# Optimization experiments

Hardware: AMD Instinct MI355X
Metric: run time of the kernel (lower is better)

Reference implementation:

```python
import jax, jax.numpy as jnp
import numpy as np
from jax import lax

DIM = 64
NUM_HEADS = 1
HEAD_DIM = DIM // NUM_HEADS
SR = 8  # reduction_ratio
SCALE = HEAD_DIM ** -0.5


def setup_inputs() -> dict:
    key = jax.random.key(0)
    ks = jax.random.split(key, 12)
    s = 0.02
    return {
        "x": jax.random.normal(ks[0], (8, 16384, DIM), dtype=jnp.float32),
        # conv sr: (out_ch, in_ch, kH, kW) torch OIHW layout
        "sr_w": jax.random.normal(ks[1], (DIM, DIM, SR, SR), dtype=jnp.float32) * s,
        "sr_b": jnp.zeros((DIM,), jnp.float32),
        "ln_g": jnp.ones((DIM,), jnp.float32),
        "ln_b": jnp.zeros((DIM,), jnp.float32),
        # torch Linear weights: (out_features, in_features)
        "q_w": jax.random.normal(ks[2], (DIM, DIM), dtype=jnp.float32) * s,
        "q_b": jnp.zeros((DIM,), jnp.float32),
        "kv_w": jax.random.normal(ks[3], (2 * DIM, DIM), dtype=jnp.float32) * s,
        "kv_b": jnp.zeros((2 * DIM,), jnp.float32),
        "proj_w": jax.random.normal(ks[4], (DIM, DIM), dtype=jnp.float32) * s,
        "proj_b": jnp.zeros((DIM,), jnp.float32),
    }


def _layernorm(x, g, b, eps=1e-5):
    mu = jnp.mean(x, axis=-1, keepdims=True)
    var = jnp.var(x, axis=-1, keepdims=True)
    return (x - mu) * lax.rsqrt(var + eps) * g + b


def reference(x, sr_w, sr_b, ln_g, ln_b, q_w, q_b, kv_w, kv_b, proj_w, proj_b):
    B, N, C = x.shape
    H = W = int(N ** 0.5)
    # q: (B, heads, N, head_dim)
    q = (x @ q_w.T + q_b).reshape(B, N, NUM_HEADS, HEAD_DIM).transpose(0, 2, 1, 3)
    # spatial reduction of KV via strided conv + LayerNorm
    x_ = x.transpose(0, 2, 1).reshape(B, C, H, W)
    x_ = lax.conv_general_dilated(
        x_, sr_w, window_strides=(SR, SR), padding="VALID",
        dimension_numbers=("NCHW", "OIHW", "NCHW"))
    x_ = x_ + sr_b[None, :, None, None]
    x_ = x_.reshape(B, C, -1).transpose(0, 2, 1)  # (B, Nr, C)
    x_ = _layernorm(x_, ln_g, ln_b)
    Nr = x_.shape[1]
    kv = (x_ @ kv_w.T + kv_b).reshape(B, Nr, 2, NUM_HEADS, HEAD_DIM)
    kv = kv.transpose(2, 0, 3, 1, 4)  # (2, B, heads, Nr, hd)
    k, v = kv[0], kv[1]
    attn = jnp.einsum("bhnd,bhmd->bhnm", q, k) * SCALE
    attn = jax.nn.softmax(attn, axis=-1)
    out = jnp.einsum("bhnm,bhmd->bhnd", attn, v)
    out = out.transpose(0, 2, 1, 3).reshape(B, N, C)
    return out @ proj_w.T + proj_b
```

## Files before the change

### kernel.cpp

```cpp
#include <hip/hip_runtime.h>


typedef __attribute__((ext_vector_type(8))) short bf16x8;
typedef __attribute__((ext_vector_type(4))) float f32x4;

__device__ __forceinline__ unsigned short f2bf(float f) {
    union { float f; unsigned int u; } a; a.f = f;
    unsigned int r = a.u + 0x7FFFu + ((a.u >> 16) & 1u);
    return (unsigned short)(r >> 16);
}
__device__ __forceinline__ float bf2f(unsigned short h) {
    union { unsigned int u; float f; } a; a.u = ((unsigned int)h) << 16;
    return a.f;
}
union U8 { uint4 u; bf16x8 v; };
__device__ __forceinline__ bf16x8 pack8(float e0,float e1,float e2,float e3,
                                        float e4,float e5,float e6,float e7){
    U8 r;
    r.u.x = (unsigned)f2bf(e0) | ((unsigned)f2bf(e1)<<16);
    r.u.y = (unsigned)f2bf(e2) | ((unsigned)f2bf(e3)<<16);
    r.u.z = (unsigned)f2bf(e4) | ((unsigned)f2bf(e5)<<16);
    r.u.w = (unsigned)f2bf(e6) | ((unsigned)f2bf(e7)<<16);
    return r.v;
}
__device__ __forceinline__ bf16x8 ldg8(const unsigned short* p){
    U8 r; r.u = *(const uint4*)p; return r.v;
}

__global__ __launch_bounds__(256) void prep_kernel(
    const float* __restrict__ sr_w, const float* __restrict__ sr_b,
    const float* __restrict__ q_w, const float* __restrict__ q_b,
    const float* __restrict__ proj_w,
    unsigned short* __restrict__ wbp, float* __restrict__ conv_out,
    unsigned short* __restrict__ qwb, unsigned short* __restrict__ pwph,
    unsigned short* __restrict__ pwpl, float* __restrict__ qb_s)
{
    int tid = blockIdx.x * 256 + threadIdx.x;
    {
        int i = tid & 7, n = (tid>>3)&15, g = (tid>>7)&3, ks = (tid>>9)&31,
            kc = (tid>>14)&3, w = tid>>16;
        int co = 16*w + n;
        int k  = kc*1024 + ks*32 + 8*g + i;
        int kh = k >> 9, kw = (k>>6)&7, cin = k & 63;
        wbp[tid] = f2bf(sr_w[co*4096 + cin*64 + kh*8 + kw]);
    }
    if (tid < 131072) conv_out[tid] = sr_b[tid & 63];
    if (tid < 4096)   qwb[tid] = f2bf(q_w[tid] * 0.125f);
    if (tid < 4096) {
        int i = tid & 7, g = (tid>>3)&3, s3 = (tid>>5)&1, co = tid>>6;
        int ch = 32*s3 + 16*(i>>2) + 4*g + (i&3);
        float w = proj_w[co*64 + ch];
        unsigned short h = f2bf(w);
        pwph[tid] = h;
        pwpl[tid] = f2bf(w - bf2f(h));
    }
    if (tid < 64) qb_s[tid] = q_b[tid] * 0.125f;
}

__global__ __launch_bounds__(256) void conv_kernel(
    const float* __restrict__ x, const unsigned short* __restrict__ wbp,
    float* __restrict__ conv_out)
{
    __shared__ char xsm[32768];
    int bid = blockIdx.x;
    int kc = bid & 3, oh = (bid>>2) & 15, b = bid >> 6;
    int t = threadIdx.x;

    const float* slab = x + ((size_t)(b*128 + oh*8 + kc*2)) * 128 * 64;
    #pragma unroll
    for (int c2 = 0; c2 < 8; ++c2) {
        int eo = (c2*256 + t) * 8;
        float4 v0 = *(const float4*)(slab + eo);
        float4 v1 = *(const float4*)(slab + eo + 4);
        int byte = eo * 2;
        int dst = byte ^ (((byte >> 10) & 7) << 4);
        U8 tmp; tmp.v = pack8(v0.x,v0.y,v0.z,v0.w,v1.x,v1.y,v1.z,v1.w);
        *(uint4*)(xsm + dst) = tmp.u;
    }
    __syncthreads();

    int w = t >> 6, lane = t & 63, g = lane >> 4, n = lane & 15;
    f32x4 acc = {0.f, 0.f, 0.f, 0.f};
    const unsigned short* wslice = wbp + (size_t)((w*4 + kc) * 32) * 512;
    int swz = (n & 7) << 4;
    #pragma unroll
    for (int ks = 0; ks < 32; ++ks) {
        bf16x8 A = ldg8(wslice + ((ks*4 + g)*16 + n) * 8);
        int byte = (ks >> 4) * 16384 + n * 1024 + ((ks & 15) * 32 + 8*g) * 2;
        U8 Bx; Bx.u = *(const uint4*)(xsm + (byte ^ swz));
        acc = __builtin_amdgcn_mfma_f32_16x16x32_bf16(A, Bx.v, acc, 0, 0, 0);
    }
    int pos = b*256 + oh*16 + n;
    int co  = 16*w + 4*g;
    #pragma unroll
    for (int r = 0; r < 4; ++r)
        atomicAdd(&conv_out[pos*64 + co + r], acc[r]);
}

__global__ __launch_bounds__(64) void lnkv_kernel(
    const float* __restrict__ conv_out,
    const float* __restrict__ ln_g, const float* __restrict__ ln_b,
    const float* __restrict__ kv_w, const float* __restrict__ kv_b,
    unsigned short* __restrict__ kbuf, unsigned short* __restrict__ vp)
{
    int gblk = blockIdx.x;
    int b = gblk >> 8, m = gblk & 255;
    int c = threadIdx.x;
    float val = conv_out[gblk*64 + c];
    float s = val, s2 = val*val;
    #pragma unroll
    for (int o = 32; o >= 1; o >>= 1) {
        s  += __shfl_xor(s,  o, 64);
        s2 += __shfl_xor(s2, o, 64);
    }
    float mean = s * (1.f/64.f);
    float var  = s2 * (1.f/64.f) - mean*mean;
    float y = (val - mean) * rsqrtf(var + 1e-5f) * ln_g[c] + ln_b[c];
    __shared__ float ys[64];
    ys[c] = y;
    __syncthreads();
    #pragma unroll
    for (int h = 0; h < 2; ++h) {
        int oc = c + h*64;
        float acc = kv_b[oc];
        const float* wr = kv_w + oc*64;
        #pragma unroll
        for (int j = 0; j < 64; j += 4) {
            float4 w4 = *(const float4*)(wr + j);
            acc += ys[j]*w4.x + ys[j+1]*w4.y + ys[j+2]*w4.z + ys[j+3]*w4.w;
        }
        if (h == 0) {
            kbuf[(b*256 + m)*64 + c] = f2bf(acc);
        } else {
            int ks = m >> 5, hi = (m >> 4) & 1, g2 = (m >> 2) & 3, r = m & 3;
            vp[(size_t)b*16384 + ((ks*4 + g2)*64 + c)*8 + r + 4*hi] = f2bf(acc);
        }
    }
}

__global__ __launch_bounds__(256) void attn_kernel(
    const float* __restrict__ x,
    const unsigned short* __restrict__ qwb, const float* __restrict__ qb_s,
    const unsigned short* __restrict__ kbuf, const unsigned short* __restrict__ vp,
    const unsigned short* __restrict__ pwph, const unsigned short* __restrict__ pwpl,
    const float* __restrict__ proj_b,
    float* __restrict__ out)
{
    __shared__ char Ks[32768];
    __shared__ char Vs[32768];
    int bid = blockIdx.x;
    int b = bid >> 8, rt = bid & 255;
    int t = threadIdx.x;
    {
        const char* kb = (const char*)(kbuf + (size_t)b*16384);
        const char* vb = (const char*)(vp   + (size_t)b*16384);
        #pragma unroll
        for (int c = 0; c < 8; ++c) {
            int off = (c*256 + t) * 16;
            int dst = off ^ (((off >> 7) & 7) << 4);
            *(uint4*)(Ks + dst) = *(const uint4*)(kb + off);
            *(uint4*)(Vs + off) = *(const uint4*)(vb + off);
        }
    }
    __syncthreads();

    int w = t >> 6, lane = t & 63, g = lane >> 4, n = lane & 15;
    int qrow = rt*64 + w*16 + n;
    const float* xr = x + ((size_t)b*16384 + qrow) * 64;

    f32x4 qacc[4];
    #pragma unroll
    for (int tau = 0; tau < 4; ++tau)
        qacc[tau] = *(const f32x4*)(qb_s + 16*tau + 4*g);
    bf16x8 xq[2];
    #pragma unroll
    for (int s = 0; s < 2; ++s) {
        float4 v0 = *(const float4*)(xr + 32*s + 8*g);
        float4 v1 = *(const float4*)(xr + 32*s + 8*g + 4);
        xq[s] = pack8(v0.x,v0.y,v0.z,v0.w,v1.x,v1.y,v1.z,v1.w);
    }
    #pragma unroll
    for (int tau = 0; tau < 4; ++tau)
        #pragma unroll
        for (int s = 0; s < 2; ++s) {
            bf16x8 A = ldg8(qwb + (16*tau + n)*64 + 32*s + 8*g);
            qacc[tau] = __builtin_amdgcn_mfma_f32_16x16x32_bf16(A, xq[s], qacc[tau], 0,0,0);
        }
    bf16x8 qkB[2];
    #pragma unroll
    for (int s2 = 0; s2 < 2; ++s2)
        qkB[s2] = pack8(qacc[2*s2][0],  qacc[2*s2][1],  qacc[2*s2][2],  qacc[2*s2][3],
                        qacc[2*s2+1][0],qacc[2*s2+1][1],qacc[2*s2+1][2],qacc[2*s2+1][3]);

    float S[16][4];
    #pragma unroll
    for (int tt = 0; tt < 16; ++tt) {
        f32x4 sa = {0.f, 0.f, 0.f, 0.f};
        int m = 16*tt + n;
        int base = m * 128;
        int swz = (m & 7) << 4;
        #pragma unroll
        for (int s2 = 0; s2 < 2; ++s2) {
            int c1 = (32*s2 + 4*g) * 2;
            uint2 d0 = *(const uint2*)(Ks + ((base + c1)      ^ swz));
            uint2 d1 = *(const uint2*)(Ks + ((base + c1 + 32) ^ swz));
            U8 A; A.u = make_uint4(d0.x, d0.y, d1.x, d1.y);
            sa = __builtin_amdgcn_mfma_f32_16x16x32_bf16(A.v, qkB[s2], sa, 0,0,0);
        }
        S[tt][0]=sa[0]; S[tt][1]=sa[1]; S[tt][2]=sa[2]; S[tt][3]=sa[3];
    }

    float rm[16];
    #pragma unroll
    for (int tt = 0; tt < 16; ++tt)
        rm[tt] = fmaxf(fmaxf(S[tt][0],S[tt][1]), fmaxf(S[tt][2],S[tt][3]));
    float m8[8];
    #pragma unroll
    for (int j = 0; j < 8; ++j) m8[j] = fmaxf(rm[2*j], rm[2*j+1]);
    float mx = fmaxf(fmaxf(fmaxf(m8[0],m8[1]),fmaxf(m8[2],m8[3])),
                     fmaxf(fmaxf(m8[4],m8[5]),fmaxf(m8[6],m8[7])));
    mx = fmaxf(mx, __shfl_xor(mx, 16, 64));
    mx = fmaxf(mx, __shfl_xor(mx, 32, 64));
    #pragma unroll
    for (int tt = 0; tt < 16; ++tt)
        #pragma unroll
        for (int r = 0; r < 4; ++r)
            S[tt][r] = __expf(S[tt][r] - mx);
    float rs[16];
    #pragma unroll
    for (int tt = 0; tt < 16; ++tt) rs[tt] = (S[tt][0]+S[tt][1]) + (S[tt][2]+S[tt][3]);
    float s8[8];
    #pragma unroll
    for (int j = 0; j < 8; ++j) s8[j] = rs[2*j] + rs[2*j+1];
    float ssum = ((s8[0]+s8[1])+(s8[2]+s8[3])) + ((s8[4]+s8[5])+(s8[6]+s8[7]));
    ssum += __shfl_xor(ssum, 16, 64);
    ssum += __shfl_xor(ssum, 32, 64);
    float inv = 1.f / ssum;

    f32x4 oacc[4] = {{0,0,0,0},{0,0,0,0},{0,0,0,0},{0,0,0,0}};
    #pragma unroll
    for (int ks = 0; ks < 8; ++ks) {
        bf16x8 Bp = pack8(S[2*ks][0]*inv,  S[2*ks][1]*inv,  S[2*ks][2]*inv,  S[2*ks][3]*inv,
                          S[2*ks+1][0]*inv,S[2*ks+1][1]*inv,S[2*ks+1][2]*inv,S[2*ks+1][3]*inv);
        #pragma unroll
        for (int tc = 0; tc < 4; ++tc) {
            U8 A; A.u = *(const uint4*)(Vs + ((ks*4 + g)*64 + 16*tc + n) * 16);
            oacc[tc] = __builtin_amdgcn_mfma_f32_16x16x32_bf16(A.v, Bp, oacc[tc], 0,0,0);
        }
    }

    U8 BhU[2], BlU[2];
    #pragma unroll
    for (int s3 = 0; s3 < 2; ++s3) {
        unsigned short hb[8], lb[8];
        #pragma unroll
        for (int j = 0; j < 8; ++j) {
            float v = oacc[2*s3 + (j>>2)][j&3];
            hb[j] = f2bf(v);
            lb[j] = f2bf(v - bf2f(hb[j]));
        }
        BhU[s3].u.x = (unsigned)hb[0] | ((unsigned)hb[1]<<16);
        BhU[s3].u.y = (unsigned)hb[2] | ((unsigned)hb[3]<<16);
        BhU[s3].u.z = (unsigned)hb[4] | ((unsigned)hb[5]<<16);
        BhU[s3].u.w = (unsigned)hb[6] | ((unsigned)hb[7]<<16);
        BlU[s3].u.x = (unsigned)lb[0] | ((unsigned)lb[1]<<16);
        BlU[s3].u.y = (unsigned)lb[2] | ((unsigned)lb[3]<<16);
        BlU[s3].u.z = (unsigned)lb[4] | ((unsigned)lb[5]<<16);
        BlU[s3].u.w = (unsigned)lb[6] | ((unsigned)lb[7]<<16);
    }
    f32x4 pacc[4];
    #pragma unroll
    for (int tf = 0; tf < 4; ++tf)
        pacc[tf] = *(const f32x4*)(proj_b + 16*tf + 4*g);
    #pragma unroll
    for (int tf = 0; tf < 4; ++tf)
        #pragma unroll
        for (int s3 = 0; s3 < 2; ++s3) {
            bf16x8 Ah = ldg8(pwph + (((16*tf + n)*2 + s3)*4 + g)*8);
            bf16x8 Al = ldg8(pwpl + (((16*tf + n)*2 + s3)*4 + g)*8);
            pacc[tf] = __builtin_amdgcn_mfma_f32_16x16x32_bf16(Ah, BhU[s3].v, pacc[tf], 0,0,0);
            pacc[tf] = __builtin_amdgcn_mfma_f32_16x16x32_bf16(Ah, BlU[s3].v, pacc[tf], 0,0,0);
            pacc[tf] = __builtin_amdgcn_mfma_f32_16x16x32_bf16(Al, BhU[s3].v, pacc[tf], 0,0,0);
        }
    float* orow = out + ((size_t)b*16384 + qrow) * 64;
    #pragma unroll
    for (int tf = 0; tf < 4; ++tf)
        *(float4*)(orow + 16*tf + 4*g) = *(float4*)&pacc[tf];
}

extern "C" void kernel_launch(void* const* d_in, const int* in_sizes, int n_in,
                              void* d_out, int out_size, void* d_ws, size_t ws_size,
                              hipStream_t stream)
{
    const float* x      = (const float*)d_in[0];
    const float* sr_w   = (const float*)d_in[1];
    const float* sr_b   = (const float*)d_in[2];
    const float* ln_g   = (const float*)d_in[3];
    const float* ln_b   = (const float*)d_in[4];
    const float* q_w    = (const float*)d_in[5];
    const float* q_b    = (const float*)d_in[6];
    const float* kv_w   = (const float*)d_in[7];
    const float* kv_b   = (const float*)d_in[8];
    const float* proj_w = (const float*)d_in[9];
    const float* proj_b = (const float*)d_in[10];
    float* out = (float*)d_out;

    char* wsb = (char*)d_ws;
    unsigned short* wbp  = (unsigned short*)(wsb);
    float*          conv = (float*)(wsb + 524288);
    unsigned short* kbuf = (unsigned short*)(wsb + 1048576);
    unsigned short* vp   = (unsigned short*)(wsb + 1310720);
    unsigned short* qwb  = (unsigned short*)(wsb + 1572864);
    unsigned short* pwph = (unsigned short*)(wsb + 1581056);
    unsigned short* pwpl = (unsigned short*)(wsb + 1589248);
    float*          qb_s = (float*)(wsb + 1597440);

    hipLaunchKernelGGL(prep_kernel, dim3(1024), dim3(256), 0, stream,
                       sr_w, sr_b, q_w, q_b, proj_w, wbp, conv, qwb, pwph, pwpl, qb_s);
    hipLaunchKernelGGL(conv_kernel, dim3(512), dim3(256), 0, stream, x, wbp, conv);
    hipLaunchKernelGGL(lnkv_kernel, dim3(2048), dim3(64), 0, stream,
                       conv, ln_g, ln_b, kv_w, kv_b, kbuf, vp);
    hipLaunchKernelGGL(attn_kernel, dim3(2048), dim3(256), 0, stream,
                       x, qwb, qb_s, kbuf, vp, pwph, pwpl, proj_b, out);
}
```

Baseline: 157.2 us.

## Drop split-bf16 projection, read V from global, enlarge attention and LN blocks

The output projection now uses a single bf16 weight and activation product instead of the three-MFMA hi/lo split, which removes two thirds of the projection MFMAs and one weight buffer. Softmax normalisation is moved from the probabilities to the attention output. V is no longer staged in shared memory but read directly from global. Attention blocks grow to 512 threads covering 128 rows, and the LN/KV kernel packs four rows per block. The risks are lower projection accuracy and more global/cache traffic for V loads.

```diff
diff --git a/kernel.cpp b/kernel.cpp
--- a/kernel.cpp
+++ b/kernel.cpp
@@ -1,17 +1,14 @@
 #include <hip/hip_runtime.h>
+#include <hip/hip_bf16.h>
 
 
 typedef __attribute__((ext_vector_type(8))) short bf16x8;
 typedef __attribute__((ext_vector_type(4))) float f32x4;
 
 __device__ __forceinline__ unsigned short f2bf(float f) {
-    union { float f; unsigned int u; } a; a.f = f;
-    unsigned int r = a.u + 0x7FFFu + ((a.u >> 16) & 1u);
-    return (unsigned short)(r >> 16);
-}
-__device__ __forceinline__ float bf2f(unsigned short h) {
-    union { unsigned int u; float f; } a; a.u = ((unsigned int)h) << 16;
-    return a.f;
+    union { __hip_bfloat16 h; unsigned short u; } cv;
+    cv.h = __hip_bfloat16(f);
+    return cv.u;
 }
 union U8 { uint4 u; bf16x8 v; };
 __device__ __forceinline__ bf16x8 pack8(float e0,float e1,float e2,float e3,
@@ -32,8 +29,8 @@
     const float* __restrict__ q_w, const float* __restrict__ q_b,
     const float* __restrict__ proj_w,
     unsigned short* __restrict__ wbp, float* __restrict__ conv_out,
-    unsigned short* __restrict__ qwb, unsigned short* __restrict__ pwph,
-    unsigned short* __restrict__ pwpl, float* __restrict__ qb_s)
+    unsigned short* __restrict__ qwb, unsigned short* __restrict__ pwp,
+    float* __restrict__ qb_s)
 {
     int tid = blockIdx.x * 256 + threadIdx.x;
     {
@@ -49,10 +46,7 @@
     if (tid < 4096) {
         int i = tid & 7, g = (tid>>3)&3, s3 = (tid>>5)&1, co = tid>>6;
         int ch = 32*s3 + 16*(i>>2) + 4*g + (i&3);
-        float w = proj_w[co*64 + ch];
-        unsigned short h = f2bf(w);
-        pwph[tid] = h;
-        pwpl[tid] = f2bf(w - bf2f(h));
+        pwp[tid] = f2bf(proj_w[co*64 + ch]);
     }
     if (tid < 64) qb_s[tid] = q_b[tid] * 0.125f;
 }
@@ -97,15 +91,15 @@
         atomicAdd(&conv_out[pos*64 + co + r], acc[r]);
 }
 
-__global__ __launch_bounds__(64) void lnkv_kernel(
+__global__ __launch_bounds__(256) void lnkv_kernel(
     const float* __restrict__ conv_out,
     const float* __restrict__ ln_g, const float* __restrict__ ln_b,
     const float* __restrict__ kv_w, const float* __restrict__ kv_b,
     unsigned short* __restrict__ kbuf, unsigned short* __restrict__ vp)
 {
-    int gblk = blockIdx.x;
+    int wv = threadIdx.x >> 6, c = threadIdx.x & 63;
+    int gblk = blockIdx.x * 4 + wv;
     int b = gblk >> 8, m = gblk & 255;
-    int c = threadIdx.x;
     float val = conv_out[gblk*64 + c];
     float s = val, s2 = val*val;
     #pragma unroll
@@ -116,8 +110,8 @@
     float mean = s * (1.f/64.f);
     float var  = s2 * (1.f/64.f) - mean*mean;
     float y = (val - mean) * rsqrtf(var + 1e-5f) * ln_g[c] + ln_b[c];
-    __shared__ float ys[64];
-    ys[c] = y;
+    __shared__ float ys[4][64];
+    ys[wv][c] = y;
     __syncthreads();
     #pragma unroll
     for (int h = 0; h < 2; ++h) {
@@ -127,7 +121,7 @@
         #pragma unroll
         for (int j = 0; j < 64; j += 4) {
             float4 w4 = *(const float4*)(wr + j);
-            acc += ys[j]*w4.x + ys[j+1]*w4.y + ys[j+2]*w4.z + ys[j+3]*w4.w;
+            acc += ys[wv][j]*w4.x + ys[wv][j+1]*w4.y + ys[wv][j+2]*w4.z + ys[wv][j+3]*w4.w;
         }
         if (h == 0) {
             kbuf[(b*256 + m)*64 + c] = f2bf(acc);
@@ -138,35 +132,32 @@
     }
 }
 
-__global__ __launch_bounds__(256) void attn_kernel(
+__global__ __launch_bounds__(512) void attn_kernel(
     const float* __restrict__ x,
     const unsigned short* __restrict__ qwb, const float* __restrict__ qb_s,
     const unsigned short* __restrict__ kbuf, const unsigned short* __restrict__ vp,
-    const unsigned short* __restrict__ pwph, const unsigned short* __restrict__ pwpl,
-    const float* __restrict__ proj_b,
+    const unsigned short* __restrict__ pwp, const float* __restrict__ proj_b,
     float* __restrict__ out)
 {
     __shared__ char Ks[32768];
-    __shared__ char Vs[32768];
     int bid = blockIdx.x;
-    int b = bid >> 8, rt = bid & 255;
+    int b = bid >> 7, rt = bid & 127;
     int t = threadIdx.x;
     {
         const char* kb = (const char*)(kbuf + (size_t)b*16384);
-        const char* vb = (const char*)(vp   + (size_t)b*16384);
-        #pragma unroll
-        for (int c = 0; c < 8; ++c) {
-            int off = (c*256 + t) * 16;
+        #pragma unroll
+        for (int c = 0; c < 4; ++c) {
+            int off = (c*512 + t) * 16;
             int dst = off ^ (((off >> 7) & 7) << 4);
             *(uint4*)(Ks + dst) = *(const uint4*)(kb + off);
-            *(uint4*)(Vs + off) = *(const uint4*)(vb + off);
         }
     }
     __syncthreads();
 
     int w = t >> 6, lane = t & 63, g = lane >> 4, n = lane & 15;
-    int qrow = rt*64 + w*16 + n;
+    int qrow = rt*128 + w*16 + n;
     const float* xr = x + ((size_t)b*16384 + qrow) * 64;
+    const char* vpb = (const char*)(vp + (size_t)b*16384);
 
     f32x4 qacc[4];
     #pragma unroll
@@ -240,34 +231,22 @@
     f32x4 oacc[4] = {{0,0,0,0},{0,0,0,0},{0,0,0,0},{0,0,0,0}};
     #pragma unroll
     for (int ks = 0; ks < 8; ++ks) {
-        bf16x8 Bp = pack8(S[2*ks][0]*inv,  S[2*ks][1]*inv,  S[2*ks][2]*inv,  S[2*ks][3]*inv,
-                          S[2*ks+1][0]*inv,S[2*ks+1][1]*inv,S[2*ks+1][2]*inv,S[2*ks+1][3]*inv);
+        bf16x8 Bp = pack8(S[2*ks][0],  S[2*ks][1],  S[2*ks][2],  S[2*ks][3],
+                          S[2*ks+1][0],S[2*ks+1][1],S[2*ks+1][2],S[2*ks+1][3]);
         #pragma unroll
         for (int tc = 0; tc < 4; ++tc) {
-            U8 A; A.u = *(const uint4*)(Vs + ((ks*4 + g)*64 + 16*tc + n) * 16);
+            U8 A; A.u = *(const uint4*)(vpb + ((ks*4 + g)*64 + 16*tc + n) * 16);
             oacc[tc] = __builtin_amdgcn_mfma_f32_16x16x32_bf16(A.v, Bp, oacc[tc], 0,0,0);
         }
     }
 
-    U8 BhU[2], BlU[2];
-    #pragma unroll
-    for (int s3 = 0; s3 < 2; ++s3) {
-        unsigned short hb[8], lb[8];
-        #pragma unroll
-        for (int j = 0; j < 8; ++j) {
-            float v = oacc[2*s3 + (j>>2)][j&3];
-            hb[j] = f2bf(v);
-            lb[j] = f2bf(v - bf2f(hb[j]));
-        }
-        BhU[s3].u.x = (unsigned)hb[0] | ((unsigned)hb[1]<<16);
-        BhU[s3].u.y = (unsigned)hb[2] | ((unsigned)hb[3]<<16);
-        BhU[s3].u.z = (unsigned)hb[4] | ((unsigned)hb[5]<<16);
-        BhU[s3].u.w = (unsigned)hb[6] | ((unsigned)hb[7]<<16);
-        BlU[s3].u.x = (unsigned)lb[0] | ((unsigned)lb[1]<<16);
-        BlU[s3].u.y = (unsigned)lb[2] | ((unsigned)lb[3]<<16);
-        BlU[s3].u.z = (unsigned)lb[4] | ((unsigned)lb[5]<<16);
-        BlU[s3].u.w = (unsigned)lb[6] | ((unsigned)lb[7]<<16);
-    }
+    bf16x8 Bo[2];
+    #pragma unroll
+    for (int s3 = 0; s3 < 2; ++s3)
+        Bo[s3] = pack8(oacc[2*s3][0]*inv,   oacc[2*s3][1]*inv,
+                       oacc[2*s3][2]*inv,   oacc[2*s3][3]*inv,
+                       oacc[2*s3+1][0]*inv, oacc[2*s3+1][1]*inv,
+                       oacc[2*s3+1][2]*inv, oacc[2*s3+1][3]*inv);
     f32x4 pacc[4];
     #pragma unroll
     for (int tf = 0; tf < 4; ++tf)
@@ -276,11 +255,8 @@
     for (int tf = 0; tf < 4; ++tf)
         #pragma unroll
         for (int s3 = 0; s3 < 2; ++s3) {
-            bf16x8 Ah = ldg8(pwph + (((16*tf + n)*2 + s3)*4 + g)*8);
-            bf16x8 Al = ldg8(pwpl + (((16*tf + n)*2 + s3)*4 + g)*8);
-            pacc[tf] = __builtin_amdgcn_mfma_f32_16x16x32_bf16(Ah, BhU[s3].v, pacc[tf], 0,0,0);
-            pacc[tf] = __builtin_amdgcn_mfma_f32_16x16x32_bf16(Ah, BlU[s3].v, pacc[tf], 0,0,0);
-            pacc[tf] = __builtin_amdgcn_mfma_f32_16x16x32_bf16(Al, BhU[s3].v, pacc[tf], 0,0,0);
+            bf16x8 Aw = ldg8(pwp + (((16*tf + n)*2 + s3)*4 + g)*8);
+            pacc[tf] = __builtin_amdgcn_mfma_f32_16x16x32_bf16(Aw, Bo[s3], pacc[tf], 0,0,0);
         }
     float* orow = out + ((size_t)b*16384 + qrow) * 64;
     #pragma unroll
@@ -311,15 +287,14 @@
     unsigned short* kbuf = (unsigned short*)(wsb + 1048576);
     unsigned short* vp   = (unsigned short*)(wsb + 1310720);
     unsigned short* qwb  = (unsigned short*)(wsb + 1572864);
-    unsigned short* pwph = (unsigned short*)(wsb + 1581056);
-    unsigned short* pwpl = (unsigned short*)(wsb + 1589248);
-    float*          qb_s = (float*)(wsb + 1597440);
+    unsigned short* pwp  = (unsigned short*)(wsb + 1581056);
+    float*          qb_s = (float*)(wsb + 1589248);
 
     hipLaunchKernelGGL(prep_kernel, dim3(1024), dim3(256), 0, stream,
-                       sr_w, sr_b, q_w, q_b, proj_w, wbp, conv, qwb, pwph, pwpl, qb_s);
+                       sr_w, sr_b, q_w, q_b, proj_w, wbp, conv, qwb, pwp, qb_s);
     hipLaunchKernelGGL(conv_kernel, dim3(512), dim3(256), 0, stream, x, wbp, conv);
-    hipLaunchKernelGGL(lnkv_kernel, dim3(2048), dim3(64), 0, stream,
+    hipLaunchKernelGGL(lnkv_kernel, dim3(512), dim3(256), 0, stream,
                        conv, ln_g, ln_b, kv_w, kv_b, kbuf, vp);
-    hipLaunchKernelGGL(attn_kernel, dim3(2048), dim3(256), 0, stream,
-                       x, qwb, qb_s, kbuf, vp, pwph, pwpl, proj_b, out);
-}
+    hipLaunchKernelGGL(attn_kernel, dim3(1024), dim3(512), 0, stream,
+                       x, qwb, qb_s, kbuf, vp, pwp, proj_b, out);
+}
```

Measured after the change: 158.2 us. About the same (+0.6%).
